# Kernel tuning notes

Hardware: AMD Instinct MI355X
Metric: run time of the kernel (lower is better)

The kernel has to match this reference:

```python
import jax, jax.numpy as jnp
import numpy as np

B, H, W, C, WS, NCLS = 8, 256, 256, 256, 8, 18


def setup_inputs() -> dict:
    key = jax.random.key(0)
    ks = jax.random.split(key, 10)
    s = 1.0 / np.sqrt(C)
    return {
        "x": jax.random.normal(ks[0], (B, H, W, C), jnp.float32),
        "Wq": jax.random.normal(ks[1], (C, NCLS), jnp.float32) * s,
        "bq": jnp.zeros((NCLS,), jnp.float32),
        "Wk": jax.random.normal(ks[2], (C, NCLS), jnp.float32) * s,
        "bk": jnp.zeros((NCLS,), jnp.float32),
        "Wv": jax.random.normal(ks[3], (C, C), jnp.float32) * s,
        "bv": jnp.zeros((C,), jnp.float32),
        "Wres": jax.random.normal(ks[4], (C, C), jnp.float32) * s,
        "bres": jnp.zeros((C,), jnp.float32),
        "gamma": jnp.zeros((1,), jnp.float32) + 0.1,
    }


def _window_partition(x):
    # (B,H,W,C) -> (B*nH*nW, ws*ws, C)
    b, h, w, c = x.shape
    x = x.reshape(b, h // WS, WS, w // WS, WS, c)
    x = jnp.transpose(x, (0, 1, 3, 2, 4, 5))
    return x.reshape(-1, WS * WS, c)


def _window_reverse(xw, c):
    # (B*nH*nW, ws*ws, c) -> (B,H,W,c)
    x = xw.reshape(B, H // WS, W // WS, WS, WS, c)
    x = jnp.transpose(x, (0, 1, 3, 2, 4, 5))
    return x.reshape(B, H, W, c)


def reference(x, Wq, bq, Wk, bk, Wv, bv, Wres, bres, gamma):
    xw = _window_partition(x)                      # (nWin, ws^2, C)
    seg_map = xw @ Wq + bq                         # (nWin, ws^2, n_cls)
    seg_ft = xw @ Wk + bk                          # (nWin, ws^2, n_cls)
    feats = xw @ Wv + bv                           # (nWin, ws^2, C)
    score = jnp.einsum('nik,njk->nij', seg_map, seg_ft)  # (nWin, ws^2, ws^2)
    score = jax.nn.softmax(score, axis=-1)
    feats = jnp.einsum('nij,njc->nic', score, feats)
    feats = feats @ Wres + bres                    # dropout = identity (eval)
    feat_map = gamma * feats + xw
    return _window_reverse(seg_map, NCLS), _window_reverse(feat_map, C)
```

## Files before the change

kernel.cpp:

```cpp
#include <hip/hip_runtime.h>
#include <hip/hip_bf16.h>


typedef __bf16 bf16_t;
typedef __bf16 bf16x8 __attribute__((ext_vector_type(8)));
typedef __bf16 bf16x4 __attribute__((ext_vector_type(4)));
typedef float  f32x4  __attribute__((ext_vector_type(4)));

#define MFMA16(a, b, c) __builtin_amdgcn_mfma_f32_16x16x32_bf16((a), (b), (c), 0, 0, 0)
#define BAR() do { asm volatile("s_waitcnt lgkmcnt(0)" ::: "memory"); \
                   __builtin_amdgcn_s_barrier(); } while (0)

static constexpr int kC = 256, kNCLS = 18;
static constexpr int WQT_OFF = 0;
static constexpr int WKT_OFF = 8192;
static constexpr int WFT_OFF = 16384;
static constexpr int BF_BYTE_OFF = 81920 * 2;

__device__ __forceinline__ int xs_i(int r, int c) { return (r << 8) + (c ^ ((r & 7) << 3)); }
__device__ __forceinline__ int sb_i(int r, int c) { return (r << 6) + (c ^ ((r & 7) << 3)); }

__global__ __launch_bounds__(256) void prep_kernel(
    const float* __restrict__ Wq, const float* __restrict__ Wk,
    const float* __restrict__ Wv, const float* __restrict__ bv,
    const float* __restrict__ Wres, const float* __restrict__ bres,
    bf16_t* __restrict__ wsb, float* __restrict__ bff)
{
  const int blk = blockIdx.x, t = threadIdx.x;
  if (blk < 256) {
    __shared__ float wcol[256];
    const int n = blk;
    wcol[t] = Wres[t * kC + n];
    __syncthreads();
    float acc = 0.f;
    const float* wvrow = Wv + (size_t)t * kC;
#pragma unroll 4
    for (int j = 0; j < 256; j += 4) {
      f32x4 a = *(const f32x4*)(wvrow + j);
      acc += a[0] * wcol[j] + a[1] * wcol[j + 1] + a[2] * wcol[j + 2] + a[3] * wcol[j + 3];
    }
    wsb[WFT_OFF + n * kC + t] = (bf16_t)acc;
  } else if (blk == 256) {
    float acc = bres[t];
    for (int j = 0; j < 256; ++j) acc += bv[j] * Wres[j * kC + t];
    bff[t] = acc;
  } else {
    int tid = (blk - 257) * 256 + t;
    if (tid < 8192) {
      int n = tid >> 8, k = tid & 255;
      wsb[WQT_OFF + tid] = (n < kNCLS) ? (bf16_t)Wq[k * kNCLS + n] : (bf16_t)0.0f;
    } else {
      int u = tid - 8192;
      int n = u >> 8, k = u & 255;
      wsb[WKT_OFF + u] = (n < kNCLS) ? (bf16_t)Wk[k * kNCLS + n] : (bf16_t)0.0f;
    }
  }
}

__global__ __launch_bounds__(256, 4) void semwin_main(
    const float* __restrict__ x,
    const float* __restrict__ bq, const float* __restrict__ bk,
    const float* __restrict__ gamma,
    const bf16_t* __restrict__ wsb, const float* __restrict__ bff,
    float* __restrict__ out0, float* __restrict__ out1)
{
  __shared__ bf16_t xsf[64 * 256];
  __shared__ bf16_t sbf[64 * 64];

  const int tid  = threadIdx.x;
  const int wave = tid >> 6;
  const int lane = tid & 63;
  const int l15  = lane & 15;
  const int g    = lane >> 4;

  const int wid = blockIdx.x;
  const int b   = wid >> 10;
  const int wh  = (wid >> 5) & 31;
  const int ww  = wid & 31;
  const int pixbase = (b << 16) + (wh << 11) + (ww << 3);

  const f32x4 fzero = {0.f, 0.f, 0.f, 0.f};
  const float gm = gamma[0];

  {
    const int t = tid >> 2;
    const int q = tid & 3;
    const float* src = x + (size_t)(pixbase + ((t >> 3) << 8) + (t & 7)) * kC + q * 8;
#pragma unroll
    for (int i = 0; i < 8; ++i) {
      f32x4 a = *(const f32x4*)(src + i * 32);
      f32x4 c = *(const f32x4*)(src + i * 32 + 4);
      bf16x8 v;
      v[0] = (bf16_t)a[0]; v[1] = (bf16_t)a[1]; v[2] = (bf16_t)a[2]; v[3] = (bf16_t)a[3];
      v[4] = (bf16_t)c[0]; v[5] = (bf16_t)c[1]; v[6] = (bf16_t)c[2]; v[7] = (bf16_t)c[3];
      *(bf16x8*)&xsf[xs_i(t, i * 32 + q * 8)] = v;
    }
  }
  BAR();

  {
    const bf16_t* wt   = wsb + ((wave < 2) ? WQT_OFF : WKT_OFF);
    const float*  bias = (wave < 2) ? bq : bk;
    const int mbase = (wave & 1) << 5;
    const int cofs  = (wave < 2) ? 0 : 32;
    f32x4 acc[2][2];
#pragma unroll
    for (int mt = 0; mt < 2; ++mt)
#pragma unroll
      for (int nt = 0; nt < 2; ++nt) acc[mt][nt] = fzero;
#pragma unroll
    for (int k0 = 0; k0 < 256; k0 += 32) {
      bf16x8 a0 = *(const bf16x8*)&xsf[xs_i(mbase + l15, k0 + g * 8)];
      bf16x8 a1 = *(const bf16x8*)&xsf[xs_i(mbase + 16 + l15, k0 + g * 8)];
      bf16x8 b0 = *(const bf16x8*)(wt + l15 * 256 + k0 + g * 8);
      bf16x8 b1 = *(const bf16x8*)(wt + (16 + l15) * 256 + k0 + g * 8);
      acc[0][0] = MFMA16(a0, b0, acc[0][0]);
      acc[0][1] = MFMA16(a0, b1, acc[0][1]);
      acc[1][0] = MFMA16(a1, b0, acc[1][0]);
      acc[1][1] = MFMA16(a1, b1, acc[1][1]);
    }
    const bool isQ = (wave < 2);
#pragma unroll
    for (int nt = 0; nt < 2; ++nt) {
      const int coln = (nt << 4) + l15;
      const float bval = (coln < kNCLS) ? bias[coln] : 0.f;
#pragma unroll
      for (int mt = 0; mt < 2; ++mt) {
#pragma unroll
        for (int r = 0; r < 4; ++r) {
          const int row = mbase + (mt << 4) + (g << 2) + r;
          const float v = acc[mt][nt][r] + bval;
          sbf[sb_i(row, cofs + coln)] = (bf16_t)v;
          if (isQ && coln < kNCLS) {
            out0[(size_t)(pixbase + ((row >> 3) << 8) + (row & 7)) * kNCLS + coln] = v;
          }
        }
      }
    }
  }
  BAR();

  {
    const int mbase = wave << 4;
    const bf16x8 aq = *(const bf16x8*)&sbf[sb_i(mbase + l15, g * 8)];
    f32x4 s[4];
#pragma unroll
    for (int nt = 0; nt < 4; ++nt) {
      bf16x8 bk8 = *(const bf16x8*)&sbf[sb_i((nt << 4) + l15, 32 + g * 8)];
      s[nt] = MFMA16(aq, bk8, fzero);
    }
    BAR();
#pragma unroll
    for (int r = 0; r < 4; ++r) {
      float m = fmaxf(fmaxf(s[0][r], s[1][r]), fmaxf(s[2][r], s[3][r]));
#pragma unroll
      for (int off = 1; off < 16; off <<= 1) m = fmaxf(m, __shfl_xor(m, off));
      float e0 = __expf(s[0][r] - m), e1 = __expf(s[1][r] - m);
      float e2 = __expf(s[2][r] - m), e3 = __expf(s[3][r] - m);
      float sum = (e0 + e1) + (e2 + e3);
#pragma unroll
      for (int off = 1; off < 16; off <<= 1) sum += __shfl_xor(sum, off);
      const float inv = 1.0f / sum;
      const int row = mbase + (g << 2) + r;
      sbf[sb_i(row, l15)]      = (bf16_t)(e0 * inv);
      sbf[sb_i(row, 16 + l15)] = (bf16_t)(e1 * inv);
      sbf[sb_i(row, 32 + l15)] = (bf16_t)(e2 * inv);
      sbf[sb_i(row, 48 + l15)] = (bf16_t)(e3 * inv);
    }
  }
  BAR();

  bf16x8 bp[4][2];
#pragma unroll
  for (int nt = 0; nt < 4; ++nt) {
    bp[nt][0] = *(const bf16x8*)&sbf[sb_i((nt << 4) + l15, g * 8)];
    bp[nt][1] = *(const bf16x8*)&sbf[sb_i((nt << 4) + l15, 32 + g * 8)];
  }
  BAR();

  for (int chunk = 0; chunk < 4; ++chunk) {
    {
      const bf16_t* wft = wsb + WFT_OFF + (size_t)((chunk << 6) + (wave << 4)) * 256;
      f32x4 accV[4];
#pragma unroll
      for (int mt = 0; mt < 4; ++mt) accV[mt] = fzero;
#pragma unroll
      for (int k0 = 0; k0 < 256; k0 += 32) {
        bf16x8 bf = *(const bf16x8*)(wft + l15 * 256 + k0 + g * 8);
#pragma unroll
        for (int mt = 0; mt < 4; ++mt) {
          bf16x8 af = *(const bf16x8*)&xsf[xs_i((mt << 4) + l15, k0 + g * 8)];
          accV[mt] = MFMA16(af, bf, accV[mt]);
        }
      }
#pragma unroll
      for (int mt = 0; mt < 4; ++mt) {
        bf16x4 pk;
#pragma unroll
        for (int r = 0; r < 4; ++r) pk[r] = (bf16_t)accV[mt][r];
        *(bf16x4*)&sbf[sb_i((wave << 4) + l15, (mt << 4) + (g << 2))] = pk;
      }
    }
    BAR();

    {
      const bf16x8 av0 = *(const bf16x8*)&sbf[sb_i((wave << 4) + l15, g * 8)];
      const bf16x8 av1 = *(const bf16x8*)&sbf[sb_i((wave << 4) + l15, 32 + g * 8)];
      const int c2 = (chunk << 6) + (wave << 4) + (g << 2);
      const f32x4 bfv = *(const f32x4*)(bff + c2);
#pragma unroll
      for (int nt = 0; nt < 4; ++nt) {
        f32x4 accC = MFMA16(av0, bp[nt][0], fzero);
        accC = MFMA16(av1, bp[nt][1], accC);
        const int t = (nt << 4) + l15;
        const bf16x4 xv = *(const bf16x4*)&xsf[xs_i(t, c2)];
        f32x4 o;
#pragma unroll
        for (int r = 0; r < 4; ++r)
          o[r] = gm * (accC[r] + bfv[r]) + (float)xv[r];
        *(f32x4*)(out1 + (size_t)(pixbase + ((t >> 3) << 8) + (t & 7)) * kC + c2) = o;
      }
    }
    if (chunk < 3) BAR();
  }
}

extern "C" void kernel_launch(void* const* d_in, const int* in_sizes, int n_in,
                              void* d_out, int out_size, void* d_ws, size_t ws_size,
                              hipStream_t stream)
{
  const float* x     = (const float*)d_in[0];
  const float* Wq    = (const float*)d_in[1];
  const float* bq    = (const float*)d_in[2];
  const float* Wk    = (const float*)d_in[3];
  const float* bk    = (const float*)d_in[4];
  const float* Wv    = (const float*)d_in[5];
  const float* bv    = (const float*)d_in[6];
  const float* Wres  = (const float*)d_in[7];
  const float* bres  = (const float*)d_in[8];
  const float* gamma = (const float*)d_in[9];
  bf16_t* wsb = (bf16_t*)d_ws;
  float*  bff = (float*)((char*)d_ws + BF_BYTE_OFF);
  float* out0 = (float*)d_out;
  float* out1 = out0 + (size_t)8 * 256 * 256 * 18;

  prep_kernel<<<dim3(321), dim3(256), 0, stream>>>(Wq, Wk, Wv, bv, Wres, bres, wsb, bff);
  semwin_main<<<dim3(8192), dim3(256), 0, stream>>>(x, bq, bk, gamma, wsb, bff, out0, out1);
}
```

Baseline: 315.8 us.

## Register-block the fused value projection over two channel chunks and drop per-chunk barriers

The per-wave value-projection loop now computes two 64-channel chunks per pass. Each x fragment read from LDS feeds MFMAs against two weight tiles, which halves the LDS reads of x in that stage. The block barriers between chunks are removed, because each wave only writes and reads its own 16 rows of the scratch buffer. In exchange each wave holds twice as many accumulators, which raises register pressure and could cost occupancy.

```diff
diff --git a/kernel.cpp b/kernel.cpp
--- a/kernel.cpp
+++ b/kernel.cpp
@@ -178,32 +178,42 @@
   }
   BAR();
 
-  for (int chunk = 0; chunk < 4; ++chunk) {
-    {
-      const bf16_t* wft = wsb + WFT_OFF + (size_t)((chunk << 6) + (wave << 4)) * 256;
-      f32x4 accV[4];
-#pragma unroll
-      for (int mt = 0; mt < 4; ++mt) accV[mt] = fzero;
-#pragma unroll
-      for (int k0 = 0; k0 < 256; k0 += 32) {
-        bf16x8 bf = *(const bf16x8*)(wft + l15 * 256 + k0 + g * 8);
-#pragma unroll
-        for (int mt = 0; mt < 4; ++mt) {
-          bf16x8 af = *(const bf16x8*)&xsf[xs_i((mt << 4) + l15, k0 + g * 8)];
-          accV[mt] = MFMA16(af, bf, accV[mt]);
-        }
-      }
+#pragma unroll
+  for (int pass = 0; pass < 2; ++pass) {
+    f32x4 accU[2][4];
+#pragma unroll
+    for (int cg = 0; cg < 2; ++cg)
+#pragma unroll
+      for (int mt = 0; mt < 4; ++mt) accU[cg][mt] = fzero;
+    const bf16_t* wft0 = wsb + WFT_OFF + (size_t)(((pass << 1) << 6) + (wave << 4) + l15) * 256;
+#pragma unroll
+    for (int k0 = 0; k0 < 256; k0 += 32) {
+      bf16x8 bf0 = *(const bf16x8*)(wft0 + k0 + g * 8);
+      bf16x8 bf1 = *(const bf16x8*)(wft0 + 64 * 256 + k0 + g * 8);
+      bf16x8 af0 = *(const bf16x8*)&xsf[xs_i(l15, k0 + g * 8)];
+      bf16x8 af1 = *(const bf16x8*)&xsf[xs_i(16 + l15, k0 + g * 8)];
+      bf16x8 af2 = *(const bf16x8*)&xsf[xs_i(32 + l15, k0 + g * 8)];
+      bf16x8 af3 = *(const bf16x8*)&xsf[xs_i(48 + l15, k0 + g * 8)];
+      accU[0][0] = MFMA16(af0, bf0, accU[0][0]);
+      accU[0][1] = MFMA16(af1, bf0, accU[0][1]);
+      accU[0][2] = MFMA16(af2, bf0, accU[0][2]);
+      accU[0][3] = MFMA16(af3, bf0, accU[0][3]);
+      accU[1][0] = MFMA16(af0, bf1, accU[1][0]);
+      accU[1][1] = MFMA16(af1, bf1, accU[1][1]);
+      accU[1][2] = MFMA16(af2, bf1, accU[1][2]);
+      accU[1][3] = MFMA16(af3, bf1, accU[1][3]);
+    }
+
+#pragma unroll
+    for (int cg = 0; cg < 2; ++cg) {
+      const int chunk = (pass << 1) + cg;
 #pragma unroll
       for (int mt = 0; mt < 4; ++mt) {
         bf16x4 pk;
 #pragma unroll
-        for (int r = 0; r < 4; ++r) pk[r] = (bf16_t)accV[mt][r];
+        for (int r = 0; r < 4; ++r) pk[r] = (bf16_t)accU[cg][mt][r];
         *(bf16x4*)&sbf[sb_i((wave << 4) + l15, (mt << 4) + (g << 2))] = pk;
       }
-    }
-    BAR();
-
-    {
       const bf16x8 av0 = *(const bf16x8*)&sbf[sb_i((wave << 4) + l15, g * 8)];
       const bf16x8 av1 = *(const bf16x8*)&sbf[sb_i((wave << 4) + l15, 32 + g * 8)];
       const int c2 = (chunk << 6) + (wave << 4) + (g << 2);
@@ -221,7 +231,6 @@
         *(f32x4*)(out1 + (size_t)(pixbase + ((t >> 3) << 8) + (t & 7)) * kC + c2) = o;
       }
     }
-    if (chunk < 3) BAR();
   }
 }
 
```

Measured after the change: 363.1 us. 1.15x slower.

## Compute each wave's full 64-channel feature slice at once and drop chunk barriers

Applied to the files above, without the earlier changes.

The value projection is restructured so each wave owns a contiguous 64-channel slice across all four 16-channel tiles, instead of looping four chunks with the waves splitting each chunk. The x fragments in LDS are loaded once per k-step and reused across four weight tiles, cutting LDS traffic. Each wave only reads back its own rows of the scratch buffer, so the block-wide barriers between chunks are removed. The cost is 64 accumulator registers held live at once, which under the launch bound of four blocks per CU may cause register pressure or spills.

```diff
diff --git a/kernel.cpp b/kernel.cpp
--- a/kernel.cpp
+++ b/kernel.cpp
@@ -178,50 +178,55 @@
   }
   BAR();
 
-  for (int chunk = 0; chunk < 4; ++chunk) {
-    {
-      const bf16_t* wft = wsb + WFT_OFF + (size_t)((chunk << 6) + (wave << 4)) * 256;
-      f32x4 accV[4];
-#pragma unroll
-      for (int mt = 0; mt < 4; ++mt) accV[mt] = fzero;
-#pragma unroll
-      for (int k0 = 0; k0 < 256; k0 += 32) {
-        bf16x8 bf = *(const bf16x8*)(wft + l15 * 256 + k0 + g * 8);
-#pragma unroll
-        for (int mt = 0; mt < 4; ++mt) {
-          bf16x8 af = *(const bf16x8*)&xsf[xs_i((mt << 4) + l15, k0 + g * 8)];
-          accV[mt] = MFMA16(af, bf, accV[mt]);
-        }
+  f32x4 accU[4][4];
+#pragma unroll
+  for (int ct = 0; ct < 4; ++ct)
+#pragma unroll
+    for (int mt = 0; mt < 4; ++mt) accU[ct][mt] = fzero;
+  {
+    const bf16_t* wftw = wsb + WFT_OFF + (size_t)((wave << 6) + l15) * 256;
+#pragma unroll
+    for (int k0 = 0; k0 < 256; k0 += 32) {
+      bf16x8 af0 = *(const bf16x8*)&xsf[xs_i(l15, k0 + g * 8)];
+      bf16x8 af1 = *(const bf16x8*)&xsf[xs_i(16 + l15, k0 + g * 8)];
+      bf16x8 af2 = *(const bf16x8*)&xsf[xs_i(32 + l15, k0 + g * 8)];
+      bf16x8 af3 = *(const bf16x8*)&xsf[xs_i(48 + l15, k0 + g * 8)];
+#pragma unroll
+      for (int ct = 0; ct < 4; ++ct) {
+        bf16x8 bf = *(const bf16x8*)(wftw + ct * 16 * 256 + k0 + g * 8);
+        accU[ct][0] = MFMA16(af0, bf, accU[ct][0]);
+        accU[ct][1] = MFMA16(af1, bf, accU[ct][1]);
+        accU[ct][2] = MFMA16(af2, bf, accU[ct][2]);
+        accU[ct][3] = MFMA16(af3, bf, accU[ct][3]);
       }
-#pragma unroll
-      for (int mt = 0; mt < 4; ++mt) {
-        bf16x4 pk;
-#pragma unroll
-        for (int r = 0; r < 4; ++r) pk[r] = (bf16_t)accV[mt][r];
-        *(bf16x4*)&sbf[sb_i((wave << 4) + l15, (mt << 4) + (g << 2))] = pk;
-      }
-    }
-    BAR();
-
-    {
-      const bf16x8 av0 = *(const bf16x8*)&sbf[sb_i((wave << 4) + l15, g * 8)];
-      const bf16x8 av1 = *(const bf16x8*)&sbf[sb_i((wave << 4) + l15, 32 + g * 8)];
-      const int c2 = (chunk << 6) + (wave << 4) + (g << 2);
-      const f32x4 bfv = *(const f32x4*)(bff + c2);
-#pragma unroll
-      for (int nt = 0; nt < 4; ++nt) {
-        f32x4 accC = MFMA16(av0, bp[nt][0], fzero);
-        accC = MFMA16(av1, bp[nt][1], accC);
-        const int t = (nt << 4) + l15;
-        const bf16x4 xv = *(const bf16x4*)&xsf[xs_i(t, c2)];
-        f32x4 o;
-#pragma unroll
-        for (int r = 0; r < 4; ++r)
-          o[r] = gm * (accC[r] + bfv[r]) + (float)xv[r];
-        *(f32x4*)(out1 + (size_t)(pixbase + ((t >> 3) << 8) + (t & 7)) * kC + c2) = o;
-      }
-    }
-    if (chunk < 3) BAR();
+    }
+  }
+
+#pragma unroll
+  for (int ct = 0; ct < 4; ++ct) {
+#pragma unroll
+    for (int mt = 0; mt < 4; ++mt) {
+      bf16x4 pk;
+#pragma unroll
+      for (int r = 0; r < 4; ++r) pk[r] = (bf16_t)accU[ct][mt][r];
+      *(bf16x4*)&sbf[sb_i((wave << 4) + l15, (mt << 4) + (g << 2))] = pk;
+    }
+    const bf16x8 av0 = *(const bf16x8*)&sbf[sb_i((wave << 4) + l15, g * 8)];
+    const bf16x8 av1 = *(const bf16x8*)&sbf[sb_i((wave << 4) + l15, 32 + g * 8)];
+    const int c2 = (wave << 6) + (ct << 4) + (g << 2);
+    const f32x4 bfv = *(const f32x4*)(bff + c2);
+#pragma unroll
+    for (int nt = 0; nt < 4; ++nt) {
+      f32x4 accC = MFMA16(av0, bp[nt][0], fzero);
+      accC = MFMA16(av1, bp[nt][1], accC);
+      const int t = (nt << 4) + l15;
+      const bf16x4 xv = *(const bf16x4*)&xsf[xs_i(t, c2)];
+      f32x4 o;
+#pragma unroll
+      for (int r = 0; r < 4; ++r)
+        o[r] = gm * (accC[r] + bfv[r]) + (float)xv[r];
+      *(f32x4*)(out1 + (size_t)(pixbase + ((t >> 3) << 8) + (t & 7)) * kC + c2) = o;
+    }
   }
 }
 
```

Measured after the change: 428.4 us. +35.6%, slower.

## Process two adjacent windows per block to reuse weight fragment loads

Applied to the files above, without the earlier changes.

Each block now handles two horizontally adjacent 8x8 windows, halving the grid and doubling LDS buffers. Weight fragments loaded from global memory (Wq/Wk and fused Wv·Wres) are reused across both windows' MFMAs, and barriers are amortized over twice the work. In exchange, LDS per block doubles to about 80KB, register pressure rises, and the launch bound drops to 2 blocks per CU, which lowers occupancy and latency hiding.

```diff
diff --git a/kernel.cpp b/kernel.cpp
--- a/kernel.cpp
+++ b/kernel.cpp
@@ -57,15 +57,17 @@
   }
 }
 
-__global__ __launch_bounds__(256, 4) void semwin_main(
+__global__ __launch_bounds__(256, 2) void semwin_main(
     const float* __restrict__ x,
     const float* __restrict__ bq, const float* __restrict__ bk,
     const float* __restrict__ gamma,
     const bf16_t* __restrict__ wsb, const float* __restrict__ bff,
     float* __restrict__ out0, float* __restrict__ out1)
 {
-  __shared__ bf16_t xsf[64 * 256];
-  __shared__ bf16_t sbf[64 * 64];
+  __shared__ bf16_t xsf0[64 * 256];
+  __shared__ bf16_t xsf1[64 * 256];
+  __shared__ bf16_t sbf0[64 * 64];
+  __shared__ bf16_t sbf1[64 * 64];
 
   const int tid  = threadIdx.x;
   const int wave = tid >> 6;
@@ -73,11 +75,12 @@
   const int l15  = lane & 15;
   const int g    = lane >> 4;
 
-  const int wid = blockIdx.x;
-  const int b   = wid >> 10;
-  const int wh  = (wid >> 5) & 31;
-  const int ww  = wid & 31;
-  const int pixbase = (b << 16) + (wh << 11) + (ww << 3);
+  const int wid2 = blockIdx.x << 1;
+  const int b    = wid2 >> 10;
+  const int wh   = (wid2 >> 5) & 31;
+  const int ww   = wid2 & 31;
+  const int pix0 = (b << 16) + (wh << 11) + (ww << 3);
+  const int pix1 = pix0 + 8;
 
   const f32x4 fzero = {0.f, 0.f, 0.f, 0.f};
   const float gm = gamma[0];
@@ -85,15 +88,23 @@
   {
     const int t = tid >> 2;
     const int q = tid & 3;
-    const float* src = x + (size_t)(pixbase + ((t >> 3) << 8) + (t & 7)) * kC + q * 8;
+    const int ro = ((t >> 3) << 8) + (t & 7);
+    const float* s0 = x + (size_t)(pix0 + ro) * kC + q * 8;
+    const float* s1 = s0 + 8 * kC;
 #pragma unroll
     for (int i = 0; i < 8; ++i) {
-      f32x4 a = *(const f32x4*)(src + i * 32);
-      f32x4 c = *(const f32x4*)(src + i * 32 + 4);
-      bf16x8 v;
-      v[0] = (bf16_t)a[0]; v[1] = (bf16_t)a[1]; v[2] = (bf16_t)a[2]; v[3] = (bf16_t)a[3];
-      v[4] = (bf16_t)c[0]; v[5] = (bf16_t)c[1]; v[6] = (bf16_t)c[2]; v[7] = (bf16_t)c[3];
-      *(bf16x8*)&xsf[xs_i(t, i * 32 + q * 8)] = v;
+      f32x4 a0 = *(const f32x4*)(s0 + i * 32);
+      f32x4 c0 = *(const f32x4*)(s0 + i * 32 + 4);
+      f32x4 a1 = *(const f32x4*)(s1 + i * 32);
+      f32x4 c1 = *(const f32x4*)(s1 + i * 32 + 4);
+      bf16x8 v0, v1;
+#pragma unroll
+      for (int r = 0; r < 4; ++r) {
+        v0[r] = (bf16_t)a0[r]; v0[4 + r] = (bf16_t)c0[r];
+        v1[r] = (bf16_t)a1[r]; v1[4 + r] = (bf16_t)c1[r];
+      }
+      *(bf16x8*)&xsf0[xs_i(t, i * 32 + q * 8)] = v0;
+      *(bf16x8*)&xsf1[xs_i(t, i * 32 + q * 8)] = v1;
     }
   }
   BAR();
@@ -103,36 +114,47 @@
     const float*  bias = (wave < 2) ? bq : bk;
     const int mbase = (wave & 1) << 5;
     const int cofs  = (wave < 2) ? 0 : 32;
-    f32x4 acc[2][2];
-#pragma unroll
-    for (int mt = 0; mt < 2; ++mt)
-#pragma unroll
-      for (int nt = 0; nt < 2; ++nt) acc[mt][nt] = fzero;
+    const bool isQ  = (wave < 2);
+    f32x4 acc[2][2][2];
+#pragma unroll
+    for (int w2 = 0; w2 < 2; ++w2)
+#pragma unroll
+      for (int mt = 0; mt < 2; ++mt)
+#pragma unroll
+        for (int nt = 0; nt < 2; ++nt) acc[w2][mt][nt] = fzero;
 #pragma unroll
     for (int k0 = 0; k0 < 256; k0 += 32) {
-      bf16x8 a0 = *(const bf16x8*)&xsf[xs_i(mbase + l15, k0 + g * 8)];
-      bf16x8 a1 = *(const bf16x8*)&xsf[xs_i(mbase + 16 + l15, k0 + g * 8)];
       bf16x8 b0 = *(const bf16x8*)(wt + l15 * 256 + k0 + g * 8);
       bf16x8 b1 = *(const bf16x8*)(wt + (16 + l15) * 256 + k0 + g * 8);
-      acc[0][0] = MFMA16(a0, b0, acc[0][0]);
-      acc[0][1] = MFMA16(a0, b1, acc[0][1]);
-      acc[1][0] = MFMA16(a1, b0, acc[1][0]);
-      acc[1][1] = MFMA16(a1, b1, acc[1][1]);
-    }
-    const bool isQ = (wave < 2);
-#pragma unroll
-    for (int nt = 0; nt < 2; ++nt) {
-      const int coln = (nt << 4) + l15;
-      const float bval = (coln < kNCLS) ? bias[coln] : 0.f;
-#pragma unroll
-      for (int mt = 0; mt < 2; ++mt) {
-#pragma unroll
-        for (int r = 0; r < 4; ++r) {
-          const int row = mbase + (mt << 4) + (g << 2) + r;
-          const float v = acc[mt][nt][r] + bval;
-          sbf[sb_i(row, cofs + coln)] = (bf16_t)v;
-          if (isQ && coln < kNCLS) {
-            out0[(size_t)(pixbase + ((row >> 3) << 8) + (row & 7)) * kNCLS + coln] = v;
+#pragma unroll
+      for (int w2 = 0; w2 < 2; ++w2) {
+        const bf16_t* xs = w2 ? xsf1 : xsf0;
+        bf16x8 a0 = *(const bf16x8*)&xs[xs_i(mbase + l15, k0 + g * 8)];
+        bf16x8 a1 = *(const bf16x8*)&xs[xs_i(mbase + 16 + l15, k0 + g * 8)];
+        acc[w2][0][0] = MFMA16(a0, b0, acc[w2][0][0]);
+        acc[w2][0][1] = MFMA16(a0, b1, acc[w2][0][1]);
+        acc[w2][1][0] = MFMA16(a1, b0, acc[w2][1][0]);
+        acc[w2][1][1] = MFMA16(a1, b1, acc[w2][1][1]);
+      }
+    }
+#pragma unroll
+    for (int w2 = 0; w2 < 2; ++w2) {
+      bf16_t* sb = w2 ? sbf1 : sbf0;
+      const int pix = w2 ? pix1 : pix0;
+#pragma unroll
+      for (int nt = 0; nt < 2; ++nt) {
+        const int coln = (nt << 4) + l15;
+        const float bval = (coln < kNCLS) ? bias[coln] : 0.f;
+#pragma unroll
+        for (int mt = 0; mt < 2; ++mt) {
+#pragma unroll
+          for (int r = 0; r < 4; ++r) {
+            const int row = mbase + (mt << 4) + (g << 2) + r;
+            const float v = acc[w2][mt][nt][r] + bval;
+            sb[sb_i(row, cofs + coln)] = (bf16_t)v;
+            if (isQ && coln < kNCLS) {
+              out0[(size_t)(pix + ((row >> 3) << 8) + (row & 7)) * kNCLS + coln] = v;
+            }
           }
         }
       }
@@ -142,83 +164,111 @@
 
   {
     const int mbase = wave << 4;
-    const bf16x8 aq = *(const bf16x8*)&sbf[sb_i(mbase + l15, g * 8)];
-    f32x4 s[4];
+    f32x4 s[2][4];
+#pragma unroll
+    for (int w2 = 0; w2 < 2; ++w2) {
+      const bf16_t* sb = w2 ? sbf1 : sbf0;
+      const bf16x8 aq = *(const bf16x8*)&sb[sb_i(mbase + l15, g * 8)];
+#pragma unroll
+      for (int nt = 0; nt < 4; ++nt) {
+        bf16x8 bk8 = *(const bf16x8*)&sb[sb_i((nt << 4) + l15, 32 + g * 8)];
+        s[w2][nt] = MFMA16(aq, bk8, fzero);
+      }
+    }
+    BAR();
+#pragma unroll
+    for (int w2 = 0; w2 < 2; ++w2) {
+      bf16_t* sb = w2 ? sbf1 : sbf0;
+#pragma unroll
+      for (int r = 0; r < 4; ++r) {
+        float m = fmaxf(fmaxf(s[w2][0][r], s[w2][1][r]), fmaxf(s[w2][2][r], s[w2][3][r]));
+#pragma unroll
+        for (int off = 1; off < 16; off <<= 1) m = fmaxf(m, __shfl_xor(m, off));
+        float e0 = __expf(s[w2][0][r] - m), e1 = __expf(s[w2][1][r] - m);
+        float e2 = __expf(s[w2][2][r] - m), e3 = __expf(s[w2][3][r] - m);
+        float sum = (e0 + e1) + (e2 + e3);
+#pragma unroll
+        for (int off = 1; off < 16; off <<= 1) sum += __shfl_xor(sum, off);
+        const float inv = 1.0f / sum;
+        const int row = mbase + (g << 2) + r;
+        sb[sb_i(row, l15)]      = (bf16_t)(e0 * inv);
+        sb[sb_i(row, 16 + l15)] = (bf16_t)(e1 * inv);
+        sb[sb_i(row, 32 + l15)] = (bf16_t)(e2 * inv);
+        sb[sb_i(row, 48 + l15)] = (bf16_t)(e3 * inv);
+      }
+    }
+  }
+  BAR();
+
+  bf16x8 bp[2][4][2];
+#pragma unroll
+  for (int w2 = 0; w2 < 2; ++w2) {
+    const bf16_t* sb = w2 ? sbf1 : sbf0;
 #pragma unroll
     for (int nt = 0; nt < 4; ++nt) {
-      bf16x8 bk8 = *(const bf16x8*)&sbf[sb_i((nt << 4) + l15, 32 + g * 8)];
-      s[nt] = MFMA16(aq, bk8, fzero);
-    }
-    BAR();
-#pragma unroll
-    for (int r = 0; r < 4; ++r) {
-      float m = fmaxf(fmaxf(s[0][r], s[1][r]), fmaxf(s[2][r], s[3][r]));
-#pragma unroll
-      for (int off = 1; off < 16; off <<= 1) m = fmaxf(m, __shfl_xor(m, off));
-      float e0 = __expf(s[0][r] - m), e1 = __expf(s[1][r] - m);
-      float e2 = __expf(s[2][r] - m), e3 = __expf(s[3][r] - m);
-      float sum = (e0 + e1) + (e2 + e3);
-#pragma unroll
-      for (int off = 1; off < 16; off <<= 1) sum += __shfl_xor(sum, off);
-      const float inv = 1.0f / sum;
-      const int row = mbase + (g << 2) + r;
-      sbf[sb_i(row, l15)]      = (bf16_t)(e0 * inv);
-      sbf[sb_i(row, 16 + l15)] = (bf16_t)(e1 * inv);
-      sbf[sb_i(row, 32 + l15)] = (bf16_t)(e2 * inv);
-      sbf[sb_i(row, 48 + l15)] = (bf16_t)(e3 * inv);
-    }
-  }
-  BAR();
-
-  bf16x8 bp[4][2];
-#pragma unroll
-  for (int nt = 0; nt < 4; ++nt) {
-    bp[nt][0] = *(const bf16x8*)&sbf[sb_i((nt << 4) + l15, g * 8)];
-    bp[nt][1] = *(const bf16x8*)&sbf[sb_i((nt << 4) + l15, 32 + g * 8)];
+      bp[w2][nt][0] = *(const bf16x8*)&sb[sb_i((nt << 4) + l15, g * 8)];
+      bp[w2][nt][1] = *(const bf16x8*)&sb[sb_i((nt << 4) + l15, 32 + g * 8)];
+    }
   }
   BAR();
 
   for (int chunk = 0; chunk < 4; ++chunk) {
     {
       const bf16_t* wft = wsb + WFT_OFF + (size_t)((chunk << 6) + (wave << 4)) * 256;
-      f32x4 accV[4];
-#pragma unroll
-      for (int mt = 0; mt < 4; ++mt) accV[mt] = fzero;
+      f32x4 accV[2][4];
+#pragma unroll
+      for (int w2 = 0; w2 < 2; ++w2)
+#pragma unroll
+        for (int mt = 0; mt < 4; ++mt) accV[w2][mt] = fzero;
 #pragma unroll
       for (int k0 = 0; k0 < 256; k0 += 32) {
         bf16x8 bf = *(const bf16x8*)(wft + l15 * 256 + k0 + g * 8);
 #pragma unroll
+        for (int w2 = 0; w2 < 2; ++w2) {
+          const bf16_t* xs = w2 ? xsf1 : xsf0;
+#pragma unroll
+          for (int mt = 0; mt < 4; ++mt) {
+            bf16x8 af = *(const bf16x8*)&xs[xs_i((mt << 4) + l15, k0 + g * 8)];
+            accV[w2][mt] = MFMA16(af, bf, accV[w2][mt]);
+          }
+        }
+      }
+#pragma unroll
+      for (int w2 = 0; w2 < 2; ++w2) {
+        bf16_t* sb = w2 ? sbf1 : sbf0;
+#pragma unroll
         for (int mt = 0; mt < 4; ++mt) {
-          bf16x8 af = *(const bf16x8*)&xsf[xs_i((mt << 4) + l15, k0 + g * 8)];
-          accV[mt] = MFMA16(af, bf, accV[mt]);
-        }
-      }
-#pragma unroll
-      for (int mt = 0; mt < 4; ++mt) {
-        bf16x4 pk;
-#pragma unroll
-        for (int r = 0; r < 4; ++r) pk[r] = (bf16_t)accV[mt][r];
-        *(bf16x4*)&sbf[sb_i((wave << 4) + l15, (mt << 4) + (g << 2))] = pk;
+          bf16x4 pk;
+#pragma unroll
+          for (int r = 0; r < 4; ++r) pk[r] = (bf16_t)accV[w2][mt][r];
+          *(bf16x4*)&sb[sb_i((wave << 4) + l15, (mt << 4) + (g << 2))] = pk;
+        }
       }
     }
     BAR();
 
     {
-      const bf16x8 av0 = *(const bf16x8*)&sbf[sb_i((wave << 4) + l15, g * 8)];
-      const bf16x8 av1 = *(const bf16x8*)&sbf[sb_i((wave << 4) + l15, 32 + g * 8)];
       const int c2 = (chunk << 6) + (wave << 4) + (g << 2);
       const f32x4 bfv = *(const f32x4*)(bff + c2);
 #pragma unroll
-      for (int nt = 0; nt < 4; ++nt) {
-        f32x4 accC = MFMA16(av0, bp[nt][0], fzero);
-        accC = MFMA16(av1, bp[nt][1], accC);
-        const int t = (nt << 4) + l15;
-        const bf16x4 xv = *(const bf16x4*)&xsf[xs_i(t, c2)];
-        f32x4 o;
-#pragma unroll
-        for (int r = 0; r < 4; ++r)
-          o[r] = gm * (accC[r] + bfv[r]) + (float)xv[r];
-        *(f32x4*)(out1 + (size_t)(pixbase + ((t >> 3) << 8) + (t & 7)) * kC + c2) = o;
+      for (int w2 = 0; w2 < 2; ++w2) {
+        const bf16_t* sb = w2 ? sbf1 : sbf0;
+        const bf16_t* xs = w2 ? xsf1 : xsf0;
+        const int pix = w2 ? pix1 : pix0;
+        const bf16x8 av0 = *(const bf16x8*)&sb[sb_i((wave << 4) + l15, g * 8)];
+        const bf16x8 av1 = *(const bf16x8*)&sb[sb_i((wave << 4) + l15, 32 + g * 8)];
+#pragma unroll
+        for (int nt = 0; nt < 4; ++nt) {
+          f32x4 accC = MFMA16(av0, bp[w2][nt][0], fzero);
+          accC = MFMA16(av1, bp[w2][nt][1], accC);
+          const int t = (nt << 4) + l15;
+          const bf16x4 xv = *(const bf16x4*)&xs[xs_i(t, c2)];
+          f32x4 o;
+#pragma unroll
+          for (int r = 0; r < 4; ++r)
+            o[r] = gm * (accC[r] + bfv[r]) + (float)xv[r];
+          *(f32x4*)(out1 + (size_t)(pix + ((t >> 3) << 8) + (t & 7)) * kC + c2) = o;
+        }
       }
     }
     if (chunk < 3) BAR();
@@ -245,5 +295,5 @@
   float* out1 = out0 + (size_t)8 * 256 * 256 * 18;
 
   prep_kernel<<<dim3(321), dim3(256), 0, stream>>>(Wq, Wk, Wv, bv, Wres, bres, wsb, bff);
-  semwin_main<<<dim3(8192), dim3(256), 0, stream>>>(x, bq, bk, gamma, wsb, bff, out0, out1);
+  semwin_main<<<dim3(4096), dim3(256), 0, stream>>>(x, bq, bk, gamma, wsb, bff, out0, out1);
 }
```

Result: faster. 301.2 us (-4.6%).
